# Kernel tuning notes

Measured on AMD Instinct MI355X. Metric: run time of the kernel, lower is better.

## Reference

```python
import jax, jax.numpy as jnp
import numpy as np

H_Q, H_KV, D_HEAD = 32, 4, 128

def setup_inputs() -> dict:
    key = jax.random.key(0)
    ks = jax.random.split(key, 5)
    B, S, H = 1, 4096, 2048
    hidden_states = jax.random.normal(ks[0], (B, S, H), jnp.float32)
    Wq = jax.random.normal(ks[1], (H, H_Q * D_HEAD), jnp.float32) * 0.02
    Wk = jax.random.normal(ks[2], (H, H_KV * D_HEAD), jnp.float32) * 0.02
    Wv = jax.random.normal(ks[3], (H, H_KV * D_HEAD), jnp.float32) * 0.02
    Wo = jax.random.normal(ks[4], (H_Q * D_HEAD, H), jnp.float32) * 0.02
    position_ids = jnp.arange(S, dtype=jnp.int32)
    # causal boolean mask, used as-is by the layer when rank != 2
    attention_mask = jnp.tril(jnp.ones((S, S), dtype=bool))[None, None]
    return dict(hidden_states=hidden_states, Wq=Wq, Wk=Wk, Wv=Wv, Wo=Wo,
                position_ids=position_ids, attention_mask=attention_mask)

def _rope(x, positions):
    # x: [B, S, H, D]; rotate-half style RoPE, max_wavelength=10000, scaling=1
    d = x.shape[-1]
    inv_freq = 1.0 / (10000.0 ** (jnp.arange(0, d, 2, dtype=jnp.float32) / d))  # [d/2]
    freq = positions.astype(jnp.float32)[:, None] * inv_freq[None, :]           # [S, d/2]
    emb = jnp.concatenate([freq, freq], axis=-1)                                # [S, d]
    cos = jnp.cos(emb)[None, :, None, :]
    sin = jnp.sin(emb)[None, :, None, :]
    x1, x2 = jnp.split(x, 2, axis=-1)
    rot = jnp.concatenate([-x2, x1], axis=-1)
    return x * cos + rot * sin

def reference(hidden_states, Wq, Wk, Wv, Wo, position_ids, attention_mask):
    B, S, H = hidden_states.shape
    q = (hidden_states @ Wq).reshape(B, S, H_Q, D_HEAD)
    k = (hidden_states @ Wk).reshape(B, S, H_KV, D_HEAD)
    v = (hidden_states @ Wv).reshape(B, S, H_KV, D_HEAD)
    q = _rope(q, position_ids)
    k = _rope(k, position_ids)
    q = q.transpose(0, 2, 1, 3)                                   # [B,Hq,S,D]
    num_groups = H_Q // H_KV
    k = jnp.repeat(k.transpose(0, 2, 1, 3), num_groups, axis=1)   # [B,Hq,S,D]
    v = jnp.repeat(v.transpose(0, 2, 1, 3), num_groups, axis=1)
    scores = jnp.einsum('bhqd,bhkd->bhqk', q, k) / jnp.sqrt(jnp.float32(D_HEAD))
    scores = jnp.where(attention_mask, scores, jnp.float32(-1e9))
    weights = jax.nn.softmax(scores, axis=-1)
    out = jnp.einsum('bhqk,bhkd->bhqd', weights, v)
    out = out.transpose(0, 2, 1, 3).reshape(B, S, H_Q * D_HEAD)
    return out @ Wo
```

## Files before the change

kernel.cpp:

```cpp
#include <hip/hip_runtime.h>
#include <hip/hip_bf16.h>

typedef __attribute__((ext_vector_type(8))) short bf16x8;
typedef __attribute__((ext_vector_type(4))) float f32x4;
typedef __attribute__((ext_vector_type(16))) float f32x16;

#define WAIT_VMCNT(n) asm volatile("s_waitcnt vmcnt(" #n ")" ::: "memory")

__device__ __forceinline__ unsigned short f2b(float f) {
  __hip_bfloat16 h = __float2bfloat16(f);
  return __builtin_bit_cast(unsigned short, h);
}
__device__ __forceinline__ float b2f(unsigned short u) {
  return __bfloat162float(__builtin_bit_cast(__hip_bfloat16, u));
}
__device__ __forceinline__ unsigned int pk2(float a, float b) {
  unsigned int r;
  asm("v_cvt_pk_bf16_f32 %0, %1, %2" : "=v"(r) : "v"(a), "v"(b));
  return r;
}

__device__ __forceinline__ void gld_lds16(const void* g, void* l) {
  __builtin_amdgcn_global_load_lds(
      (const __attribute__((address_space(1))) unsigned int*)g,
      (__attribute__((address_space(3))) unsigned int*)l, 16, 0, 0);
}

__global__ void convert_kernel(const float* __restrict__ in, unsigned short* __restrict__ out, int n4) {
  int i = blockIdx.x * blockDim.x + threadIdx.x;
  if (i >= n4) return;
  float4 v = ((const float4*)in)[i];
  uint2 o;
  o.x = pk2(v.x, v.y);
  o.y = pk2(v.z, v.w);
  *(uint2*)(out + (size_t)i * 4) = o;
}

__global__ void transpose_convert_kernel(const float* __restrict__ in, unsigned short* __restrict__ out,
                                         int R, int C) {
  __shared__ float tile[32][33];
  int c0 = blockIdx.x * 32, r0 = blockIdx.y * 32;
  int tx = threadIdx.x, ty = threadIdx.y;
#pragma unroll
  for (int k = 0; k < 32; k += 8)
    tile[ty + k][tx] = in[(size_t)(r0 + ty + k) * C + (c0 + tx)];
  __syncthreads();
#pragma unroll
  for (int k = 0; k < 32; k += 8)
    out[(size_t)(c0 + ty + k) * R + (r0 + tx)] = f2b(tile[tx][ty + k]);
}

__global__ void rope_kernel(unsigned short* __restrict__ buf, const int* __restrict__ pos,
                            int log2h, int rowstride, float outscale, int total) {
  int idx = blockIdx.x * blockDim.x + threadIdx.x;
  if (idx >= total) return;
  int i = idx & 63;
  int h = (idx >> 6) & ((1 << log2h) - 1);
  int s = idx >> (6 + log2h);
  float inv = expf(-0.14391156831212787f * (float)i);
  float f = (float)pos[s] * inv;
  float sn, cs;
  sincosf(f, &sn, &cs);
  unsigned short* p = buf + (size_t)s * rowstride + (h << 7) + i;
  float x1 = b2f(p[0]);
  float x2 = b2f(p[64]);
  p[0]  = f2b((x1 * cs - x2 * sn) * outscale);
  p[64] = f2b((x2 * cs + x1 * sn) * outscale);
}

template <int OUT_MODE>
__global__ __launch_bounds__(256) void gemm_bt_kernel(const unsigned short* __restrict__ A,
                                                      const unsigned short* __restrict__ Bt,
                                                      void* __restrict__ Cv,
                                                      void* __restrict__ C1,
                                                      void* __restrict__ C2,
                                                      int M, int N, int K) {
  __shared__ unsigned short As[3][128 * 32];
  __shared__ unsigned short Bs[3][128 * 32];
  int tid = threadIdx.x;
  int lane = tid & 63;
  int wave = tid >> 6;

  int nwg = gridDim.x * gridDim.y;
  int lin = blockIdx.y * gridDim.x + blockIdx.x;
  int cpx = nwg >> 3;
  int swz = (lin & 7) * cpx + (lin >> 3);
  int m0 = (swz / gridDim.x) * 128, n0 = (swz % gridDim.x) * 128;

  int wr = wave >> 1, wc = wave & 1;
  f32x4 acc[4][4] = {};

  int row0 = tid >> 2, cc0 = tid & 3;
  const unsigned short* pa0 = A + (size_t)(m0 + row0) * K + cc0 * 8;
  const unsigned short* pa1 = A + (size_t)(m0 + row0 + 64) * K + cc0 * 8;
  const unsigned short* pb0 = Bt + (size_t)(n0 + row0) * K + cc0 * 8;
  const unsigned short* pb1 = Bt + (size_t)(n0 + row0 + 64) * K + cc0 * 8;

  auto stage = [&](int b, int k0) {
    gld_lds16(pa0 + k0, (unsigned short*)As[b] + tid * 8);
    gld_lds16(pa1 + k0, (unsigned short*)As[b] + (256 + tid) * 8);
    gld_lds16(pb0 + k0, (unsigned short*)Bs[b] + tid * 8);
    gld_lds16(pb1 + k0, (unsigned short*)Bs[b] + (256 + tid) * 8);
  };

  int nk = K >> 5;
  stage(0, 0);
  stage(1, 32);
  int cur = 0;
  for (int ki = 0; ki < nk; ++ki) {
    if (ki + 1 < nk) WAIT_VMCNT(4); else WAIT_VMCNT(0);
    __builtin_amdgcn_s_barrier();
    if (ki + 2 < nk) {
      int b2 = cur + 2; if (b2 >= 3) b2 -= 3;
      stage(b2, (ki + 2) * 32);
    }
    bf16x8 af[4], bfr[4];
#pragma unroll
    for (int mi = 0; mi < 4; ++mi) {
      int r = wr * 64 + mi * 16 + (lane & 15);
      af[mi] = *(const bf16x8*)((const char*)As[cur] + r * 64 + (lane >> 4) * 16);
    }
#pragma unroll
    for (int ni = 0; ni < 4; ++ni) {
      int r = wc * 64 + ni * 16 + (lane & 15);
      bfr[ni] = *(const bf16x8*)((const char*)Bs[cur] + r * 64 + (lane >> 4) * 16);
    }
#pragma unroll
    for (int mi = 0; mi < 4; ++mi)
#pragma unroll
      for (int ni = 0; ni < 4; ++ni)
        acc[mi][ni] = __builtin_amdgcn_mfma_f32_16x16x32_bf16(af[mi], bfr[ni], acc[mi][ni], 0, 0, 0);
    cur = (cur == 2) ? 0 : cur + 1;
  }

#pragma unroll
  for (int mi = 0; mi < 4; ++mi) {
#pragma unroll
    for (int ni = 0; ni < 4; ++ni) {
      int col = n0 + wc * 64 + ni * 16 + (lane & 15);
      int rbase = m0 + wr * 64 + mi * 16 + (lane >> 4) * 4;
      if (OUT_MODE == 1) {
#pragma unroll
        for (int j = 0; j < 4; ++j)
          ((float*)Cv)[(size_t)(rbase + j) * N + col] = acc[mi][ni][j];
      } else {
        if (n0 < 4096) {
#pragma unroll
          for (int j = 0; j < 4; ++j)
            ((unsigned short*)Cv)[(size_t)(rbase + j) * 4096 + col] = f2b(acc[mi][ni][j]);
        } else if (n0 < 4608) {
          int c2 = col - 4096;
#pragma unroll
          for (int j = 0; j < 4; ++j)
            ((unsigned short*)C1)[(size_t)(rbase + j) * 512 + c2] = f2b(acc[mi][ni][j]);
        } else {
          int cv = col - 4608;
          int hk = cv >> 7, d = cv & 127;
          uint2 u;
          u.x = pk2(acc[mi][ni][0], acc[mi][ni][1]);
          u.y = pk2(acc[mi][ni][2], acc[mi][ni][3]);
          size_t addr = (size_t)hk * 524288 + (size_t)(rbase >> 6) * 8192 + d * 64 + (rbase & 63);
          *(uint2*)((unsigned short*)C2 + addr) = u;
        }
      }
    }
  }
}

__global__ __launch_bounds__(512) void attn_kernel(const unsigned short* __restrict__ Q,
                                                   const unsigned short* __restrict__ Kp,
                                                   const unsigned short* __restrict__ Vt,
                                                   unsigned short* __restrict__ O) {
  __shared__ unsigned short k_lds[3][64 * 128];
  __shared__ unsigned short vt_lds[3][128 * 64];

  int lin = blockIdx.y * 8 + blockIdx.x;
  int h = (lin & 7) * 4 + (lin >> 6);
  int xpair = (lin >> 3) & 7;
  int hk = h >> 3;
  int tid = threadIdx.x, lane = tid & 63, wave = tid >> 6;
  int l31 = lane & 31, hi = lane >> 5;

  int krow0 = tid >> 4, kch = tid & 15;
  int krow1 = krow0 + 32;
  const unsigned short* kp0 = Kp + (hk << 7) + (size_t)krow0 * 512 + ((kch ^ (krow0 & 15)) << 3);
  const unsigned short* kp1 = Kp + (hk << 7) + (size_t)krow1 * 512 + ((kch ^ (krow1 & 15)) << 3);
  int vd0 = tid >> 3, vsc = tid & 7;
  int vd1 = vd0 + 64;
  const unsigned short* vp0 = Vt + (size_t)hk * 524288 + vd0 * 64 + ((vsc ^ (vd0 & 7)) << 3);
  const unsigned short* vp1 = Vt + (size_t)hk * 524288 + vd1 * 64 + ((vsc ^ (vd1 & 7)) << 3);

  auto stage_tile = [&](int b, int t) {
    gld_lds16(kp0 + t * 32768, (unsigned short*)k_lds[b] + tid * 8);
    gld_lds16(kp1 + t * 32768, (unsigned short*)k_lds[b] + (512 + tid) * 8);
    gld_lds16(vp0 + t * 8192, (unsigned short*)vt_lds[b] + tid * 8);
    gld_lds16(vp1 + t * 8192, (unsigned short*)vt_lds[b] + (512 + tid) * 8);
  };

  for (int pass = 0; pass < 2; ++pass) {
    int SB = pass ? (15 - xpair) : xpair;
    int qt = SB * 8 + wave;
    int qrow = qt * 32 + l31;
    int tdiag = qt >> 1;
    int ntiles = 4 * SB + 4;

    bf16x8 qf[8];
#pragma unroll
    for (int kk = 0; kk < 8; ++kk)
      qf[kk] = *(const bf16x8*)(Q + (size_t)qrow * 4096 + (h << 7) + kk * 16 + hi * 8);

    f32x16 o_acc[4] = {};
    float m_run = -3.0e38f, l_run = 0.0f;

    __syncthreads();
    stage_tile(0, 0);
    stage_tile(1, 1);
    int cur = 0;
    for (int t0 = 0; t0 < ntiles; ++t0) {
      if (t0 + 1 < ntiles) WAIT_VMCNT(4); else WAIT_VMCNT(0);
      __builtin_amdgcn_s_barrier();
      if (t0 + 2 < ntiles) {
        int b2 = cur + 2; if (b2 >= 3) b2 -= 3;
        stage_tile(b2, t0 + 2);
      }

      if (t0 <= tdiag) {
        int s0 = t0 * 64;
        f32x16 sacc[2] = {};
        __builtin_amdgcn_s_setprio(1);
#pragma unroll
        for (int kk = 0; kk < 8; ++kk) {
#pragma unroll
          for (int t = 0; t < 2; ++t) {
            bf16x8 kf = *(const bf16x8*)((const char*)k_lds[cur] +
                         ((t * 32 + l31) * 256 + (((kk * 2 + hi) ^ (l31 & 15)) << 4)));
            sacc[t] = __builtin_amdgcn_mfma_f32_32x32x16_bf16(kf, qf[kk], sacc[t], 0, 0, 0);
          }
        }
        __builtin_amdgcn_s_setprio(0);

        float mx = -3.0e38f;
        if (t0 == tdiag) {
#pragma unroll
          for (int t = 0; t < 2; ++t)
#pragma unroll
            for (int r = 0; r < 16; ++r) {
              int sg = s0 + t * 32 + (r & 3) + 8 * (r >> 2) + 4 * hi;
              float v = sacc[t][r];
              v = (sg <= qrow) ? v : -3.0e38f;
              sacc[t][r] = v;
              mx = fmaxf(mx, v);
            }
        } else {
#pragma unroll
          for (int t = 0; t < 2; ++t)
#pragma unroll
            for (int r = 0; r < 16; ++r)
              mx = fmaxf(mx, sacc[t][r]);
        }
        mx = fmaxf(mx, __shfl_xor(mx, 32));
        if (!__all(mx <= m_run + 11.5416f)) {
          float m_new = fmaxf(m_run, mx);
          float corr = exp2f(m_run - m_new);
          l_run *= corr;
#pragma unroll
          for (int ds = 0; ds < 4; ++ds)
#pragma unroll
            for (int r = 0; r < 16; ++r) o_acc[ds][r] *= corr;
          m_run = m_new;
        }
        float rsum = 0.0f;
#pragma unroll
        for (int t = 0; t < 2; ++t)
#pragma unroll
          for (int r = 0; r < 16; ++r) {
            float e = exp2f(sacc[t][r] - m_run);
            sacc[t][r] = e;
            rsum += e;
          }
        l_run += rsum + __shfl_xor(rsum, 32);

        bf16x8 pb[4];
#pragma unroll
        for (int kk = 0; kk < 4; ++kk) {
          int t = kk >> 1;
          int b0 = (kk & 1) * 8;
          unsigned int a0 = pk2(sacc[t][b0 + 0], sacc[t][b0 + 1]);
          unsigned int a1 = pk2(sacc[t][b0 + 2], sacc[t][b0 + 3]);
          unsigned int c0 = pk2(sacc[t][b0 + 4], sacc[t][b0 + 5]);
          unsigned int c1 = pk2(sacc[t][b0 + 6], sacc[t][b0 + 7]);
          unsigned int snd0 = hi ? a0 : c0, snd1 = hi ? a1 : c1;
          unsigned int rcv0 = __shfl_xor(snd0, 32);
          unsigned int rcv1 = __shfl_xor(snd1, 32);
          unsigned int own0 = hi ? c0 : a0, own1 = hi ? c1 : a1;
          uint4 w;
          w.x = hi ? rcv0 : own0;
          w.y = hi ? rcv1 : own1;
          w.z = hi ? own0 : rcv0;
          w.w = hi ? own1 : rcv1;
          pb[kk] = __builtin_bit_cast(bf16x8, w);
        }

        __builtin_amdgcn_s_setprio(1);
#pragma unroll
        for (int ds = 0; ds < 4; ++ds) {
#pragma unroll
          for (int kk = 0; kk < 4; ++kk) {
            bf16x8 vf = *(const bf16x8*)((const char*)vt_lds[cur] +
                         ((ds * 32 + l31) * 128 + (((kk * 2 + hi) ^ (l31 & 7)) << 4)));
            o_acc[ds] = __builtin_amdgcn_mfma_f32_32x32x16_bf16(vf, pb[kk], o_acc[ds], 0, 0, 0);
          }
        }
        __builtin_amdgcn_s_setprio(0);
      }
      cur = (cur == 2) ? 0 : cur + 1;
    }

    __syncthreads();

    float inv_l = 1.0f / l_run;
    char* scr = (char*)k_lds + wave * 2304;
#pragma unroll
    for (int ds = 0; ds < 4; ++ds) {
#pragma unroll
      for (int rp = 0; rp < 8; ++rp) {
        int r = rp * 2;
        int d_loc = (r & 3) + 8 * (r >> 2) + 4 * hi;
        *(unsigned int*)(scr + l31 * 72 + ((d_loc >> 1) << 2)) =
            pk2(o_acc[ds][r] * inv_l, o_acc[ds][r + 1] * inv_l);
      }
      uint2 u0 = *(uint2*)(scr + l31 * 72 + hi * 32 + 0);
      uint2 u1 = *(uint2*)(scr + l31 * 72 + hi * 32 + 8);
      uint2 u2 = *(uint2*)(scr + l31 * 72 + hi * 32 + 16);
      uint2 u3 = *(uint2*)(scr + l31 * 72 + hi * 32 + 24);
      unsigned short* op = O + (size_t)qrow * 4096 + (h << 7) + ds * 32 + hi * 16;
      uint4 s0v; s0v.x = u0.x; s0v.y = u0.y; s0v.z = u1.x; s0v.w = u1.y;
      uint4 s1v; s1v.x = u2.x; s1v.y = u2.y; s1v.z = u3.x; s1v.w = u3.y;
      *(uint4*)(op) = s0v;
      *(uint4*)(op + 8) = s1v;
    }
  }
}

extern "C" void kernel_launch(void* const* d_in, const int* in_sizes, int n_in,
                              void* d_out, int out_size, void* d_ws, size_t ws_size,
                              hipStream_t stream) {
  const float* X  = (const float*)d_in[0];
  const float* Wq = (const float*)d_in[1];
  const float* Wk = (const float*)d_in[2];
  const float* Wv = (const float*)d_in[3];
  const float* Wo = (const float*)d_in[4];
  const int* pos  = (const int*)d_in[5];

  const size_t MB = 1u << 20;
  char* w = (char*)d_ws;
  unsigned short* Xb  = (unsigned short*)(w + 0 * MB);
  unsigned short* Wqt = (unsigned short*)(w + 16 * MB);
  unsigned short* Wkt = (unsigned short*)(w + 32 * MB);
  unsigned short* Wvt = (unsigned short*)(w + 34 * MB);
  unsigned short* Wot = (unsigned short*)(w + 36 * MB);
  unsigned short* Qb  = (unsigned short*)(w + 52 * MB);
  unsigned short* Kb  = (unsigned short*)(w + 84 * MB);
  unsigned short* Vtb = (unsigned short*)(w + 88 * MB);
  unsigned short* Ob  = (unsigned short*)(w + 92 * MB);

  convert_kernel<<<8192, 256, 0, stream>>>(X, Xb, 4096 * 2048 / 4);
  transpose_convert_kernel<<<dim3(128, 64), dim3(32, 8), 0, stream>>>(Wq, Wqt, 2048, 4096);
  transpose_convert_kernel<<<dim3(16, 64),  dim3(32, 8), 0, stream>>>(Wk, Wkt, 2048, 512);
  transpose_convert_kernel<<<dim3(16, 64),  dim3(32, 8), 0, stream>>>(Wv, Wvt, 2048, 512);
  transpose_convert_kernel<<<dim3(64, 128), dim3(32, 8), 0, stream>>>(Wo, Wot, 4096, 2048);

  gemm_bt_kernel<3><<<dim3(40, 32), 256, 0, stream>>>(Xb, Wqt, Qb, Kb, Vtb, 4096, 5120, 2048);

  rope_kernel<<<(4096 * 32 * 64) / 256, 256, 0, stream>>>(Qb, pos, 5, 4096, 0.12752792534390558f, 4096 * 32 * 64);
  rope_kernel<<<(4096 * 4 * 64) / 256,  256, 0, stream>>>(Kb, pos, 2, 512, 1.0f, 4096 * 4 * 64);

  attn_kernel<<<dim3(8, 32), 512, 0, stream>>>(Qb, Kb, Vtb, Ob);

  gemm_bt_kernel<1><<<dim3(16, 32), 256, 0, stream>>>(Ob, Wot, d_out, nullptr, nullptr, 4096, 2048, 4096);
}
```

Measured before the change: 445.3 us.

## Split attention KV tiles across two blocks and merge partial outputs

The attention grid is doubled: each block handles the even or odd KV tiles for its query group and writes an unnormalized bf16 partial output plus its running max and sum. A new combine kernel merges the two partials using the log-sum-exp weights. The per-block LDS ring goes from triple to double buffering, with an extra barrier, and launch bounds request higher occupancy. The aim is to fill more CUs during the causal attention phase, at the cost of an extra kernel, extra memory traffic and bf16 rounding of the partials before they are merged.

```diff
diff --git a/kernel.cpp b/kernel.cpp
--- a/kernel.cpp
+++ b/kernel.cpp
@@ -6,6 +6,7 @@
 typedef __attribute__((ext_vector_type(16))) float f32x16;
 
 #define WAIT_VMCNT(n) asm volatile("s_waitcnt vmcnt(" #n ")" ::: "memory")
+#define WAIT_LGKM0()  asm volatile("s_waitcnt lgkmcnt(0)" ::: "memory")
 
 __device__ __forceinline__ unsigned short f2b(float f) {
   __hip_bfloat16 h = __float2bfloat16(f);
@@ -167,16 +168,22 @@
   }
 }
 
-__global__ __launch_bounds__(512) void attn_kernel(const unsigned short* __restrict__ Q,
-                                                   const unsigned short* __restrict__ Kp,
-                                                   const unsigned short* __restrict__ Vt,
-                                                   unsigned short* __restrict__ O) {
-  __shared__ unsigned short k_lds[3][64 * 128];
-  __shared__ unsigned short vt_lds[3][128 * 64];
-
-  int lin = blockIdx.y * 8 + blockIdx.x;
-  int h = (lin & 7) * 4 + (lin >> 6);
-  int xpair = (lin >> 3) & 7;
+__global__ __launch_bounds__(512, 4) void attn_kernel(const unsigned short* __restrict__ Q,
+                                                      const unsigned short* __restrict__ Kp,
+                                                      const unsigned short* __restrict__ Vt,
+                                                      unsigned short* __restrict__ p0,
+                                                      unsigned short* __restrict__ p1,
+                                                      float2* __restrict__ ml) {
+  __shared__ unsigned short k_lds[2][64 * 128];
+  __shared__ unsigned short vt_lds[2][128 * 64];
+
+  int lin = blockIdx.x;
+  int xcd = lin & 7;
+  int h = xcd * 4 + ((lin >> 3) & 3);
+  int xpair = (lin >> 5) & 7;
+  int half = lin >> 8;
+  unsigned short* P = half ? p1 : p0;
+
   int hk = h >> 3;
   int tid = threadIdx.x, lane = tid & 63, wave = tid >> 6;
   int l31 = lane & 31, hi = lane >> 5;
@@ -190,11 +197,12 @@
   const unsigned short* vp0 = Vt + (size_t)hk * 524288 + vd0 * 64 + ((vsc ^ (vd0 & 7)) << 3);
   const unsigned short* vp1 = Vt + (size_t)hk * 524288 + vd1 * 64 + ((vsc ^ (vd1 & 7)) << 3);
 
-  auto stage_tile = [&](int b, int t) {
-    gld_lds16(kp0 + t * 32768, (unsigned short*)k_lds[b] + tid * 8);
-    gld_lds16(kp1 + t * 32768, (unsigned short*)k_lds[b] + (512 + tid) * 8);
-    gld_lds16(vp0 + t * 8192, (unsigned short*)vt_lds[b] + tid * 8);
-    gld_lds16(vp1 + t * 8192, (unsigned short*)vt_lds[b] + (512 + tid) * 8);
+  auto stage_tile = [&](int b, int iloc) {
+    int t = 2 * iloc + half;
+    gld_lds16(kp0 + (size_t)t * 32768, (unsigned short*)k_lds[b] + tid * 8);
+    gld_lds16(kp1 + (size_t)t * 32768, (unsigned short*)k_lds[b] + (512 + tid) * 8);
+    gld_lds16(vp0 + (size_t)t * 8192, (unsigned short*)vt_lds[b] + tid * 8);
+    gld_lds16(vp1 + (size_t)t * 8192, (unsigned short*)vt_lds[b] + (512 + tid) * 8);
   };
 
   for (int pass = 0; pass < 2; ++pass) {
@@ -202,7 +210,7 @@
     int qt = SB * 8 + wave;
     int qrow = qt * 32 + l31;
     int tdiag = qt >> 1;
-    int ntiles = 4 * SB + 4;
+    int nloc = 2 * SB + 2;
 
     bf16x8 qf[8];
 #pragma unroll
@@ -215,17 +223,14 @@
     __syncthreads();
     stage_tile(0, 0);
     stage_tile(1, 1);
-    int cur = 0;
-    for (int t0 = 0; t0 < ntiles; ++t0) {
-      if (t0 + 1 < ntiles) WAIT_VMCNT(4); else WAIT_VMCNT(0);
+    for (int i = 0; i < nloc; ++i) {
+      int cur = i & 1;
+      if (i + 1 < nloc) WAIT_VMCNT(4); else WAIT_VMCNT(0);
       __builtin_amdgcn_s_barrier();
-      if (t0 + 2 < ntiles) {
-        int b2 = cur + 2; if (b2 >= 3) b2 -= 3;
-        stage_tile(b2, t0 + 2);
-      }
-
-      if (t0 <= tdiag) {
-        int s0 = t0 * 64;
+
+      int t0g = 2 * i + half;
+      if (t0g <= tdiag) {
+        int s0 = t0g * 64;
         f32x16 sacc[2] = {};
         __builtin_amdgcn_s_setprio(1);
 #pragma unroll
@@ -240,7 +245,7 @@
         __builtin_amdgcn_s_setprio(0);
 
         float mx = -3.0e38f;
-        if (t0 == tdiag) {
+        if (t0g == tdiag) {
 #pragma unroll
           for (int t = 0; t < 2; ++t)
 #pragma unroll
@@ -313,12 +318,13 @@
         }
         __builtin_amdgcn_s_setprio(0);
       }
-      cur = (cur == 2) ? 0 : cur + 1;
+      WAIT_LGKM0();
+      __builtin_amdgcn_s_barrier();
+      if (i + 2 < nloc) stage_tile(cur, i + 2);
     }
 
     __syncthreads();
 
-    float inv_l = 1.0f / l_run;
     char* scr = (char*)k_lds + wave * 2304;
 #pragma unroll
     for (int ds = 0; ds < 4; ++ds) {
@@ -327,19 +333,53 @@
         int r = rp * 2;
         int d_loc = (r & 3) + 8 * (r >> 2) + 4 * hi;
         *(unsigned int*)(scr + l31 * 72 + ((d_loc >> 1) << 2)) =
-            pk2(o_acc[ds][r] * inv_l, o_acc[ds][r + 1] * inv_l);
+            pk2(o_acc[ds][r], o_acc[ds][r + 1]);
       }
       uint2 u0 = *(uint2*)(scr + l31 * 72 + hi * 32 + 0);
       uint2 u1 = *(uint2*)(scr + l31 * 72 + hi * 32 + 8);
       uint2 u2 = *(uint2*)(scr + l31 * 72 + hi * 32 + 16);
       uint2 u3 = *(uint2*)(scr + l31 * 72 + hi * 32 + 24);
-      unsigned short* op = O + (size_t)qrow * 4096 + (h << 7) + ds * 32 + hi * 16;
+      unsigned short* op = P + (size_t)qrow * 4096 + (h << 7) + ds * 32 + hi * 16;
       uint4 s0v; s0v.x = u0.x; s0v.y = u0.y; s0v.z = u1.x; s0v.w = u1.y;
       uint4 s1v; s1v.x = u2.x; s1v.y = u2.y; s1v.z = u3.x; s1v.w = u3.y;
       *(uint4*)(op) = s0v;
       *(uint4*)(op + 8) = s1v;
     }
+    if (hi == 0)
+      ml[(size_t)(half * 32 + h) * 4096 + qrow] = make_float2(m_run, l_run);
   }
+}
+
+__global__ void combine_kernel(const unsigned short* p0,
+                               const unsigned short* __restrict__ p1,
+                               const float2* __restrict__ ml,
+                               unsigned short* out) {
+  int i = blockIdx.x * 256 + threadIdx.x;
+  size_t base = (size_t)i * 8;
+  int q = (int)(base >> 12);
+  int h = ((int)base & 4095) >> 7;
+  float2 a = ml[(size_t)h * 4096 + q];
+  float2 b = ml[(size_t)(32 + h) * 4096 + q];
+  float m = fmaxf(a.x, b.x);
+  float w0 = exp2f(a.x - m);
+  float w1 = exp2f(b.x - m);
+  float inv = 1.0f / (a.y * w0 + b.y * w1);
+  w0 *= inv; w1 *= inv;
+  uint4 u0 = *(const uint4*)(p0 + base);
+  uint4 u1 = *(const uint4*)(p1 + base);
+  uint4 o;
+  unsigned int* pu0 = (unsigned int*)&u0;
+  unsigned int* pu1 = (unsigned int*)&u1;
+  unsigned int* po = (unsigned int*)&o;
+#pragma unroll
+  for (int k = 0; k < 4; ++k) {
+    float lo = b2f((unsigned short)(pu0[k] & 0xffffu)) * w0 +
+               b2f((unsigned short)(pu1[k] & 0xffffu)) * w1;
+    float hv = b2f((unsigned short)(pu0[k] >> 16)) * w0 +
+               b2f((unsigned short)(pu1[k] >> 16)) * w1;
+    po[k] = pk2(lo, hv);
+  }
+  *(uint4*)(out + base) = o;
 }
 
 extern "C" void kernel_launch(void* const* d_in, const int* in_sizes, int n_in,
@@ -363,6 +403,8 @@
   unsigned short* Kb  = (unsigned short*)(w + 84 * MB);
   unsigned short* Vtb = (unsigned short*)(w + 88 * MB);
   unsigned short* Ob  = (unsigned short*)(w + 92 * MB);
+  unsigned short* P1  = (unsigned short*)(w + 0 * MB);
+  float2* ML          = (float2*)(w + 34 * MB);
 
   convert_kernel<<<8192, 256, 0, stream>>>(X, Xb, 4096 * 2048 / 4);
   transpose_convert_kernel<<<dim3(128, 64), dim3(32, 8), 0, stream>>>(Wq, Wqt, 2048, 4096);
@@ -375,7 +417,9 @@
   rope_kernel<<<(4096 * 32 * 64) / 256, 256, 0, stream>>>(Qb, pos, 5, 4096, 0.12752792534390558f, 4096 * 32 * 64);
   rope_kernel<<<(4096 * 4 * 64) / 256,  256, 0, stream>>>(Kb, pos, 2, 512, 1.0f, 4096 * 4 * 64);
 
-  attn_kernel<<<dim3(8, 32), 512, 0, stream>>>(Qb, Kb, Vtb, Ob);
+  attn_kernel<<<512, 512, 0, stream>>>(Qb, Kb, Vtb, Ob, P1, ML);
+
+  combine_kernel<<<8192, 256, 0, stream>>>(Ob, P1, ML, Ob);
 
   gemm_bt_kernel<1><<<dim3(16, 32), 256, 0, stream>>>(Ob, Wot, d_out, nullptr, nullptr, 4096, 2048, 4096);
 }
```

After: 623.1 us. 39.9% more time.

## Replace 128x128 GEMM with 256-row tiled, swizzled-LDS, 512-thread GEMM kernel

Applied to the files above, without the earlier changes.

Both projection GEMMs move from a 128x128x32 tile with 256 threads and triple buffering to a 256xBN x64 tile with 512 threads (8 waves) and double buffering. The LDS layout is XOR-swizzled to avoid bank conflicts, and a second barrier after the LDS reads lets the next stage reuse the current buffer. The MFMA block is wrapped in raised wave priority. The aim is higher arithmetic intensity per tile and fewer LDS conflicts, at the cost of more registers and LDS per block and fewer workgroups (320 and 256) to fill the CUs.

```diff
diff --git a/kernel.cpp b/kernel.cpp
--- a/kernel.cpp
+++ b/kernel.cpp
@@ -6,6 +6,7 @@
 typedef __attribute__((ext_vector_type(16))) float f32x16;
 
 #define WAIT_VMCNT(n) asm volatile("s_waitcnt vmcnt(" #n ")" ::: "memory")
+#define WAIT_LGKM0()  asm volatile("s_waitcnt lgkmcnt(0)" ::: "memory")
 
 __device__ __forceinline__ unsigned short f2b(float f) {
   __hip_bfloat16 h = __float2bfloat16(f);
@@ -68,87 +69,106 @@
   p[64] = f2b((x2 * cs + x1 * sn) * outscale);
 }
 
-template <int OUT_MODE>
-__global__ __launch_bounds__(256) void gemm_bt_kernel(const unsigned short* __restrict__ A,
-                                                      const unsigned short* __restrict__ Bt,
-                                                      void* __restrict__ Cv,
-                                                      void* __restrict__ C1,
-                                                      void* __restrict__ C2,
-                                                      int M, int N, int K) {
-  __shared__ unsigned short As[3][128 * 32];
-  __shared__ unsigned short Bs[3][128 * 32];
-  int tid = threadIdx.x;
-  int lane = tid & 63;
-  int wave = tid >> 6;
-
-  int nwg = gridDim.x * gridDim.y;
-  int lin = blockIdx.y * gridDim.x + blockIdx.x;
-  int cpx = nwg >> 3;
-  int swz = (lin & 7) * cpx + (lin >> 3);
-  int m0 = (swz / gridDim.x) * 128, n0 = (swz % gridDim.x) * 128;
-
-  int wr = wave >> 1, wc = wave & 1;
-  f32x4 acc[4][4] = {};
-
-  int row0 = tid >> 2, cc0 = tid & 3;
-  const unsigned short* pa0 = A + (size_t)(m0 + row0) * K + cc0 * 8;
-  const unsigned short* pa1 = A + (size_t)(m0 + row0 + 64) * K + cc0 * 8;
-  const unsigned short* pb0 = Bt + (size_t)(n0 + row0) * K + cc0 * 8;
-  const unsigned short* pb1 = Bt + (size_t)(n0 + row0 + 64) * K + cc0 * 8;
-
-  auto stage = [&](int b, int k0) {
-    gld_lds16(pa0 + k0, (unsigned short*)As[b] + tid * 8);
-    gld_lds16(pa1 + k0, (unsigned short*)As[b] + (256 + tid) * 8);
-    gld_lds16(pb0 + k0, (unsigned short*)Bs[b] + tid * 8);
-    gld_lds16(pb1 + k0, (unsigned short*)Bs[b] + (256 + tid) * 8);
+template <int OUT_MODE, int BN>
+__global__ __launch_bounds__(512, 2) void gemm256_kernel(const unsigned short* __restrict__ A,
+                                                         const unsigned short* __restrict__ Bt,
+                                                         void* __restrict__ Cv,
+                                                         void* __restrict__ C1,
+                                                         void* __restrict__ C2,
+                                                         int M, int N, int K) {
+  constexpr int WN = BN / 4;
+  constexpr int NI = WN / 16;
+  constexpr int B_IT = BN * 8 / 512;
+  __shared__ unsigned short As[2][256 * 64];
+  __shared__ unsigned short Bs[2][BN * 64];
+
+  int tid = threadIdx.x, lane = tid & 63, wave = tid >> 6;
+  int wm = wave >> 2, wn = wave & 3;
+
+  int gx = gridDim.x, nwg = gx * gridDim.y;
+  int lin = blockIdx.y * gx + blockIdx.x;
+  int swz = (lin & 7) * (nwg >> 3) + (lin >> 3);
+  int m0 = (swz / gx) * 256, n0 = (swz % gx) * BN;
+
+  int row0 = tid >> 3, ch = tid & 7;
+  const unsigned short* pa0 = A + (size_t)(m0 + row0) * K + ((ch ^ (row0 & 7)) << 3);
+  const unsigned short* pb0 = Bt + (size_t)(n0 + row0) * K + ((ch ^ (row0 & 7)) << 3);
+  size_t rstep = (size_t)64 * K;
+
+  auto stage = [&](int b, int kt) {
+    const unsigned short* a = pa0 + (size_t)kt * 64;
+    const unsigned short* bb = pb0 + (size_t)kt * 64;
+#pragma unroll
+    for (int it = 0; it < 4; ++it)
+      gld_lds16(a + it * rstep, (unsigned short*)As[b] + (it * 512 + tid) * 8);
+#pragma unroll
+    for (int it = 0; it < B_IT; ++it)
+      gld_lds16(bb + it * rstep, (unsigned short*)Bs[b] + (it * 512 + tid) * 8);
   };
 
-  int nk = K >> 5;
+  f32x4 acc[8][NI] = {};
+
+  int nk = K >> 6;
   stage(0, 0);
-  stage(1, 32);
-  int cur = 0;
-  for (int ki = 0; ki < nk; ++ki) {
-    if (ki + 1 < nk) WAIT_VMCNT(4); else WAIT_VMCNT(0);
+  stage(1, 1);
+  for (int kt = 0; kt < nk; ++kt) {
+    int cur = kt & 1;
+    if (kt + 1 < nk) {
+      if constexpr (BN == 256) WAIT_VMCNT(8); else WAIT_VMCNT(6);
+    } else {
+      WAIT_VMCNT(0);
+    }
     __builtin_amdgcn_s_barrier();
-    if (ki + 2 < nk) {
-      int b2 = cur + 2; if (b2 >= 3) b2 -= 3;
-      stage(b2, (ki + 2) * 32);
-    }
-    bf16x8 af[4], bfr[4];
-#pragma unroll
-    for (int mi = 0; mi < 4; ++mi) {
-      int r = wr * 64 + mi * 16 + (lane & 15);
-      af[mi] = *(const bf16x8*)((const char*)As[cur] + r * 64 + (lane >> 4) * 16);
-    }
-#pragma unroll
-    for (int ni = 0; ni < 4; ++ni) {
-      int r = wc * 64 + ni * 16 + (lane & 15);
-      bfr[ni] = *(const bf16x8*)((const char*)Bs[cur] + r * 64 + (lane >> 4) * 16);
-    }
-#pragma unroll
-    for (int mi = 0; mi < 4; ++mi)
-#pragma unroll
-      for (int ni = 0; ni < 4; ++ni)
-        acc[mi][ni] = __builtin_amdgcn_mfma_f32_16x16x32_bf16(af[mi], bfr[ni], acc[mi][ni], 0, 0, 0);
-    cur = (cur == 2) ? 0 : cur + 1;
+
+    bf16x8 af[8][2], bfr[NI][2];
+#pragma unroll
+    for (int mi = 0; mi < 8; ++mi) {
+      int r = wm * 128 + mi * 16 + (lane & 15);
+#pragma unroll
+      for (int kk = 0; kk < 2; ++kk)
+        af[mi][kk] = *(const bf16x8*)((const char*)As[cur] +
+                      r * 128 + (((kk * 4 + (lane >> 4)) ^ (r & 7)) << 4));
+    }
+#pragma unroll
+    for (int ni = 0; ni < NI; ++ni) {
+      int r = wn * WN + ni * 16 + (lane & 15);
+#pragma unroll
+      for (int kk = 0; kk < 2; ++kk)
+        bfr[ni][kk] = *(const bf16x8*)((const char*)Bs[cur] +
+                       r * 128 + (((kk * 4 + (lane >> 4)) ^ (r & 7)) << 4));
+    }
+    WAIT_LGKM0();
+    __builtin_amdgcn_s_barrier();
+    if (kt + 2 < nk) stage(cur, kt + 2);
+
+    __builtin_amdgcn_s_setprio(1);
+#pragma unroll
+    for (int mi = 0; mi < 8; ++mi)
+#pragma unroll
+      for (int ni = 0; ni < NI; ++ni)
+#pragma unroll
+        for (int kk = 0; kk < 2; ++kk)
+          acc[mi][ni] = __builtin_amdgcn_mfma_f32_16x16x32_bf16(af[mi][kk], bfr[ni][kk],
+                                                                acc[mi][ni], 0, 0, 0);
+    __builtin_amdgcn_s_setprio(0);
   }
 
 #pragma unroll
-  for (int mi = 0; mi < 4; ++mi) {
-#pragma unroll
-    for (int ni = 0; ni < 4; ++ni) {
-      int col = n0 + wc * 64 + ni * 16 + (lane & 15);
-      int rbase = m0 + wr * 64 + mi * 16 + (lane >> 4) * 4;
+  for (int mi = 0; mi < 8; ++mi) {
+#pragma unroll
+    for (int ni = 0; ni < NI; ++ni) {
+      int col = n0 + wn * WN + ni * 16 + (lane & 15);
+      int rbase = m0 + wm * 128 + mi * 16 + (lane >> 4) * 4;
       if (OUT_MODE == 1) {
 #pragma unroll
         for (int j = 0; j < 4; ++j)
           ((float*)Cv)[(size_t)(rbase + j) * N + col] = acc[mi][ni][j];
       } else {
-        if (n0 < 4096) {
+        if (col < 4096) {
 #pragma unroll
           for (int j = 0; j < 4; ++j)
             ((unsigned short*)Cv)[(size_t)(rbase + j) * 4096 + col] = f2b(acc[mi][ni][j]);
-        } else if (n0 < 4608) {
+        } else if (col < 4608) {
           int c2 = col - 4096;
 #pragma unroll
           for (int j = 0; j < 4; ++j)
@@ -191,10 +211,10 @@
   const unsigned short* vp1 = Vt + (size_t)hk * 524288 + vd1 * 64 + ((vsc ^ (vd1 & 7)) << 3);
 
   auto stage_tile = [&](int b, int t) {
-    gld_lds16(kp0 + t * 32768, (unsigned short*)k_lds[b] + tid * 8);
-    gld_lds16(kp1 + t * 32768, (unsigned short*)k_lds[b] + (512 + tid) * 8);
-    gld_lds16(vp0 + t * 8192, (unsigned short*)vt_lds[b] + tid * 8);
-    gld_lds16(vp1 + t * 8192, (unsigned short*)vt_lds[b] + (512 + tid) * 8);
+    gld_lds16(kp0 + (size_t)t * 32768, (unsigned short*)k_lds[b] + tid * 8);
+    gld_lds16(kp1 + (size_t)t * 32768, (unsigned short*)k_lds[b] + (512 + tid) * 8);
+    gld_lds16(vp0 + (size_t)t * 8192, (unsigned short*)vt_lds[b] + tid * 8);
+    gld_lds16(vp1 + (size_t)t * 8192, (unsigned short*)vt_lds[b] + (512 + tid) * 8);
   };
 
   for (int pass = 0; pass < 2; ++pass) {
@@ -370,12 +390,12 @@
   transpose_convert_kernel<<<dim3(16, 64),  dim3(32, 8), 0, stream>>>(Wv, Wvt, 2048, 512);
   transpose_convert_kernel<<<dim3(64, 128), dim3(32, 8), 0, stream>>>(Wo, Wot, 4096, 2048);
 
-  gemm_bt_kernel<3><<<dim3(40, 32), 256, 0, stream>>>(Xb, Wqt, Qb, Kb, Vtb, 4096, 5120, 2048);
+  gemm256_kernel<3, 256><<<dim3(20, 16), 512, 0, stream>>>(Xb, Wqt, Qb, Kb, Vtb, 4096, 5120, 2048);
 
   rope_kernel<<<(4096 * 32 * 64) / 256, 256, 0, stream>>>(Qb, pos, 5, 4096, 0.12752792534390558f, 4096 * 32 * 64);
   rope_kernel<<<(4096 * 4 * 64) / 256,  256, 0, stream>>>(Kb, pos, 2, 512, 1.0f, 4096 * 4 * 64);
 
   attn_kernel<<<dim3(8, 32), 512, 0, stream>>>(Qb, Kb, Vtb, Ob);
 
-  gemm_bt_kernel<1><<<dim3(16, 32), 256, 0, stream>>>(Ob, Wot, d_out, nullptr, nullptr, 4096, 2048, 4096);
-}
+  gemm256_kernel<1, 128><<<dim3(16, 16), 512, 0, stream>>>(Ob, Wot, d_out, nullptr, nullptr, 4096, 2048, 4096);
+}
```

New measurement: 437.2 us. No clear change (-1.8%).
